# Optimization experiments

Hardware: AMD Instinct MI355X
Metric: run time of the kernel (lower is better)

The kernel has to match this reference:

```python
import jax, jax.numpy as jnp
import numpy as np

NUM_CLASSES = 512


def setup_inputs() -> dict:
    key = jax.random.key(0)
    k1, k2 = jax.random.split(key)
    support_data = jax.random.normal(k1, (2560, 64, 5, 5), dtype=jnp.float32)
    query_data = jax.random.normal(k2, (8192, 64, 5, 5), dtype=jnp.float32)
    # every class 0..511 appears exactly 5 times (sorted, like unique() ordering)
    support_label = (jnp.arange(2560, dtype=jnp.int32) // 5).astype(jnp.int32)
    return {"support_data": support_data, "query_data": query_data,
            "support_label": support_label}


def reference(support_data, query_data, support_label):
    # embedding_net == identity: embeddings are the raw (N, C, H, W) tensors.
    n_q = query_data.shape[0]
    d = support_data.shape[1] * support_data.shape[2] * support_data.shape[3]
    s = support_data.reshape(support_data.shape[0], d)   # [Ns, d]
    q = query_data.reshape(n_q, d)                        # [Nq, d]

    # class-mean prototypes (scatter-mean == per-unique-label mean loop)
    sums = jax.ops.segment_sum(s, support_label, num_segments=NUM_CLASSES)      # [M, d]
    counts = jax.ops.segment_sum(jnp.ones((s.shape[0],), s.dtype),
                                 support_label, num_segments=NUM_CLASSES)       # [M]
    protos = sums / counts[:, None]                                             # [M, d]

    # squared euclidean distance: ||q||^2 + ||p||^2 - 2 q.p  (same math as
    # broadcast (q - p)**2 summed over c,h,w, without the [Nq,M,d] intermediate)
    q2 = jnp.sum(q * q, axis=1, keepdims=True)            # [Nq, 1]
    p2 = jnp.sum(protos * protos, axis=1)                 # [M]
    dist = q2 + p2[None, :] - 2.0 * (q @ protos.T)        # [Nq, M]

    return jax.nn.log_softmax(-dist, axis=1)
```

## Files before the change

### kernel.cpp

```cpp
#include <hip/hip_runtime.h>
#include <hip/hip_bf16.h>
#include <cstdint>
#include <cstddef>

#define NS 2560
#define NQ 8192
#define NC 512
#define DD 1600

typedef __bf16 bf16_t;
typedef __bf16 bf16x4 __attribute__((ext_vector_type(4)));
typedef __bf16 bf16x8 __attribute__((ext_vector_type(8)));
typedef float f32x4 __attribute__((ext_vector_type(4)));

__global__ __launch_bounds__(256) void proto_kernel(
    const float* __restrict__ sup, const int* __restrict__ lab,
    bf16_t* __restrict__ protos, float* __restrict__ p2)
{
    const int m   = blockIdx.x;
    const int tid = threadIdx.x;
    __shared__ int   idxs[32];
    __shared__ int   cnt;
    __shared__ float wsum[4];
    if (tid == 0) cnt = 0;
    __syncthreads();
    for (int i = tid; i < NS; i += 256) {
        if (lab[i] == m) {
            int p = atomicAdd(&cnt, 1);
            if (p < 32) idxs[p] = i;
        }
    }
    __syncthreads();
    int n = cnt < 32 ? cnt : 32;
    if (tid == 0 && n > 1) {
        for (int a = 1; a < n; ++a) {
            int key = idxs[a]; int b = a - 1;
            while (b >= 0 && idxs[b] > key) { idxs[b+1] = idxs[b]; --b; }
            idxs[b+1] = key;
        }
    }
    __syncthreads();

    float acc[7];
    #pragma unroll
    for (int u = 0; u < 7; ++u) acc[u] = 0.f;
    for (int t = 0; t < n; ++t) {
        const float* src = sup + (size_t)idxs[t] * DD;
        #pragma unroll
        for (int u = 0; u < 7; ++u) {
            int j = tid + u * 256;
            if (j < DD) acc[u] += src[j];
        }
    }
    float inv = (n > 0) ? 1.f / (float)n : 0.f;
    float psq = 0.f;
    #pragma unroll
    for (int u = 0; u < 7; ++u) {
        int j = tid + u * 256;
        if (j < DD) {
            float p = acc[u] * inv;
            bf16_t pb = (bf16_t)p;
            protos[(size_t)m * DD + j] = pb;
            float pf = (float)pb;
            psq += pf * pf;
        }
    }
    #pragma unroll
    for (int o = 32; o > 0; o >>= 1) psq += __shfl_xor(psq, o);
    int lane = tid & 63, wid = tid >> 6;
    if (lane == 0) wsum[wid] = psq;
    __syncthreads();
    if (tid == 0) p2[m] = wsum[0] + wsum[1] + wsum[2] + wsum[3];
}

__device__ __forceinline__ void stage_B(const bf16_t* __restrict__ pb,
                                        char* bbuf, int k0, int tid, int wid)
{
    #pragma unroll
    for (int p = 0; p < 4; ++p) {
        int idx  = p * 256 + tid;
        int row  = idx >> 3;
        int gcol = (idx & 7) ^ (row & 7);
        const bf16_t* src = pb + (size_t)row * DD + k0 + gcol * 8;
        char* dst = bbuf + (size_t)(p * 256 + wid * 64) * 16;
        __builtin_amdgcn_global_load_lds(
            (const __attribute__((address_space(1))) void*)src,
            (__attribute__((address_space(3))) void*)dst, 16, 0, 0);
    }
}

__global__ __launch_bounds__(256, 4) void gemm_kernel(
    const float* __restrict__ q, const bf16_t* __restrict__ protos,
    const float* __restrict__ p2, float* __restrict__ out)
{
    __shared__ char smem[20480];

    const int tid  = threadIdx.x;
    const int lane = tid & 63;
    const int wid  = tid >> 6;
    const int r    = lane & 15;
    const int g    = lane >> 4;
    const int m0   = blockIdx.x * 32;
    const int n0   = blockIdx.y * 128;

    const bf16_t* pb = protos + (size_t)n0 * DD;

    float p2c[2];
    #pragma unroll
    for (int ni = 0; ni < 2; ++ni) p2c[ni] = p2[n0 + wid * 32 + ni * 16 + r];

    f32x4 acc[2][2];
    #pragma unroll
    for (int mi = 0; mi < 2; ++mi)
        #pragma unroll
        for (int ni = 0; ni < 2; ++ni)
            acc[mi][ni] = (f32x4){0.f, 0.f, 0.f, 0.f};

    const int ar0 = tid >> 4, ac0 = tid & 15;
    const int ar1 = (256 + tid) >> 4, ac1 = tid & 15;
    const float* ap0 = q + (size_t)(m0 + ar0) * DD + ac0 * 4;
    const float* ap1 = q + (size_t)(m0 + ar1) * DD + ac1 * 4;
    const int ao0 = (ar0 * 128 + ac0 * 8) ^ ((ar0 & 7) << 4);
    const int ao1 = (ar1 * 128 + ac1 * 8) ^ ((ar1 & 7) << 4);

    char* Bs = smem;
    char* As = smem + 16384;

    for (int t = 0; t < 25; ++t) {
        float4 f0 = *(const float4*)(ap0 + t * 64);
        float4 f1 = *(const float4*)(ap1 + t * 64);
        stage_B(pb, Bs, t * 64, tid, wid);
        bf16x4 w0, w1;
        w0[0] = (bf16_t)f0.x; w0[1] = (bf16_t)f0.y;
        w0[2] = (bf16_t)f0.z; w0[3] = (bf16_t)f0.w;
        w1[0] = (bf16_t)f1.x; w1[1] = (bf16_t)f1.y;
        w1[2] = (bf16_t)f1.z; w1[3] = (bf16_t)f1.w;
        *(bf16x4*)(As + ao0) = w0;
        *(bf16x4*)(As + ao1) = w1;
        __syncthreads();

        #pragma unroll
        for (int kk = 0; kk < 2; ++kk) {
            bf16x8 af[2], bfr[2];
            #pragma unroll
            for (int mi = 0; mi < 2; ++mi) {
                int a_r = mi * 16 + r;
                int ab  = (a_r * 128 + kk * 64 + g * 16) ^ ((a_r & 7) << 4);
                af[mi] = *(const bf16x8*)(As + ab);
            }
            #pragma unroll
            for (int ni = 0; ni < 2; ++ni) {
                int c  = wid * 32 + ni * 16 + r;
                int bb = (c * 128 + kk * 64 + g * 16) ^ ((c & 7) << 4);
                bfr[ni] = *(const bf16x8*)(Bs + bb);
            }
            #pragma unroll
            for (int mi = 0; mi < 2; ++mi)
                #pragma unroll
                for (int ni = 0; ni < 2; ++ni)
                    acc[mi][ni] = __builtin_amdgcn_mfma_f32_16x16x32_bf16(
                        af[mi], bfr[ni], acc[mi][ni], 0, 0, 0);
        }
        __syncthreads();
    }

    #pragma unroll
    for (int mi = 0; mi < 2; ++mi) {
        #pragma unroll
        for (int j = 0; j < 4; ++j) {
            size_t rowoff = (size_t)(m0 + mi * 16 + g * 4 + j) * NC + n0;
            #pragma unroll
            for (int ni = 0; ni < 2; ++ni)
                out[rowoff + wid * 32 + ni * 16 + r] =
                    2.f * acc[mi][ni][j] - p2c[ni];
        }
    }
}

__global__ __launch_bounds__(256) void lsm_kernel(float* __restrict__ io)
{
    const int row  = blockIdx.x * 4 + (threadIdx.x >> 6);
    const int lane = threadIdx.x & 63;
    float* p = io + (size_t)row * NC + lane * 8;

    float4 a = *(const float4*)(p);
    float4 b = *(const float4*)(p + 4);
    float v[8] = {a.x, a.y, a.z, a.w, b.x, b.y, b.z, b.w};

    float mx = v[0];
    #pragma unroll
    for (int i = 1; i < 8; ++i) mx = fmaxf(mx, v[i]);
    #pragma unroll
    for (int o = 32; o > 0; o >>= 1) mx = fmaxf(mx, __shfl_xor(mx, o));
    float se = 0.f;
    #pragma unroll
    for (int i = 0; i < 8; ++i) se += expf(v[i] - mx);
    #pragma unroll
    for (int o = 32; o > 0; o >>= 1) se += __shfl_xor(se, o);
    float lz = mx + logf(se);

    float4 o1 = {v[0]-lz, v[1]-lz, v[2]-lz, v[3]-lz};
    float4 o2 = {v[4]-lz, v[5]-lz, v[6]-lz, v[7]-lz};
    *(float4*)(p)     = o1;
    *(float4*)(p + 4) = o2;
}

extern "C" void kernel_launch(void* const* d_in, const int* in_sizes, int n_in,
                              void* d_out, int out_size, void* d_ws, size_t ws_size,
                              hipStream_t stream)
{
    const float* sup = (const float*)d_in[0];
    const float* qry = (const float*)d_in[1];
    const int*   lab = (const int*)d_in[2];
    float* out = (float*)d_out;

    char* ws = (char*)d_ws;
    bf16_t* protos = (bf16_t*)ws;
    float*  p2     = (float*)(ws + 1638400);

    proto_kernel<<<NC, 256, 0, stream>>>(sup, lab, protos, p2);
    gemm_kernel<<<dim3(NQ / 32, 4), 256, 0, stream>>>(qry, protos, p2, out);
    lsm_kernel<<<NQ / 4, 256, 0, stream>>>(out);
}
```

Before: 57.45 us.

## Enlarge GEMM tile to 128x128 with 8 waves and double-buffered LDS prefetch

The GEMM block tile grows from 32x128 to 128x128 using 512 threads arranged as 2x4 waves, each computing a 64x32 sub-tile. This cuts how often the prototype tiles are re-read from global memory. A double-buffered LDS pipeline is added: the next K-slice of A (fp32 converted to bf16) and B (async global_load_lds) is issued before the current slice's MFMAs, so only one barrier per iteration remains. In exchange it uses 64KB of dynamic shared memory and a grid of only 256 blocks, which lowers occupancy and may underfill the CUs.

After: 59.32 us. 3.3% more time.

```diff
diff --git a/kernel.cpp b/kernel.cpp
--- a/kernel.cpp
+++ b/kernel.cpp
@@ -77,101 +77,132 @@
                                         char* bbuf, int k0, int tid, int wid)
 {
     #pragma unroll
-    for (int p = 0; p < 4; ++p) {
-        int idx  = p * 256 + tid;
+    for (int p = 0; p < 2; ++p) {
+        int idx  = p * 512 + tid;
         int row  = idx >> 3;
         int gcol = (idx & 7) ^ (row & 7);
         const bf16_t* src = pb + (size_t)row * DD + k0 + gcol * 8;
-        char* dst = bbuf + (size_t)(p * 256 + wid * 64) * 16;
+        char* dst = bbuf + (size_t)(p * 512 + wid * 64) * 16;
         __builtin_amdgcn_global_load_lds(
             (const __attribute__((address_space(1))) void*)src,
             (__attribute__((address_space(3))) void*)dst, 16, 0, 0);
     }
 }
 
-__global__ __launch_bounds__(256, 4) void gemm_kernel(
+__global__ __launch_bounds__(512, 2) void gemm_kernel(
     const float* __restrict__ q, const bf16_t* __restrict__ protos,
     const float* __restrict__ p2, float* __restrict__ out)
 {
-    __shared__ char smem[20480];
+    extern __shared__ char smem[];
 
     const int tid  = threadIdx.x;
     const int lane = tid & 63;
     const int wid  = tid >> 6;
+    const int wm   = wid >> 2;
+    const int wn   = wid & 3;
     const int r    = lane & 15;
     const int g    = lane >> 4;
-    const int m0   = blockIdx.x * 32;
+    const int m0   = blockIdx.x * 128;
     const int n0   = blockIdx.y * 128;
 
     const bf16_t* pb = protos + (size_t)n0 * DD;
 
     float p2c[2];
     #pragma unroll
-    for (int ni = 0; ni < 2; ++ni) p2c[ni] = p2[n0 + wid * 32 + ni * 16 + r];
-
-    f32x4 acc[2][2];
-    #pragma unroll
-    for (int mi = 0; mi < 2; ++mi)
+    for (int ni = 0; ni < 2; ++ni) p2c[ni] = p2[n0 + wn * 32 + ni * 16 + r];
+
+    f32x4 acc[4][2];
+    #pragma unroll
+    for (int mi = 0; mi < 4; ++mi)
         #pragma unroll
         for (int ni = 0; ni < 2; ++ni)
             acc[mi][ni] = (f32x4){0.f, 0.f, 0.f, 0.f};
 
-    const int ar0 = tid >> 4, ac0 = tid & 15;
-    const int ar1 = (256 + tid) >> 4, ac1 = tid & 15;
-    const float* ap0 = q + (size_t)(m0 + ar0) * DD + ac0 * 4;
-    const float* ap1 = q + (size_t)(m0 + ar1) * DD + ac1 * 4;
-    const int ao0 = (ar0 * 128 + ac0 * 8) ^ ((ar0 & 7) << 4);
-    const int ao1 = (ar1 * 128 + ac1 * 8) ^ ((ar1 & 7) << 4);
-
-    char* Bs = smem;
-    char* As = smem + 16384;
+    const int acg = tid & 15;
+    int          arow[4];
+    const float* ap[4];
+    int          ao[4];
+    #pragma unroll
+    for (int u = 0; u < 4; ++u) {
+        arow[u] = (u * 512 + tid) >> 4;
+        ap[u]   = q + (size_t)(m0 + arow[u]) * DD + acg * 4;
+        ao[u]   = (arow[u] * 128 + acg * 8) ^ ((arow[u] & 7) << 4);
+    }
+
+    {
+        float4 f[4];
+        #pragma unroll
+        for (int u = 0; u < 4; ++u) f[u] = *(const float4*)(ap[u]);
+        stage_B(pb, smem, 0, tid, wid);
+        #pragma unroll
+        for (int u = 0; u < 4; ++u) {
+            bf16x4 w;
+            w[0] = (bf16_t)f[u].x; w[1] = (bf16_t)f[u].y;
+            w[2] = (bf16_t)f[u].z; w[3] = (bf16_t)f[u].w;
+            *(bf16x4*)(smem + 32768 + ao[u]) = w;
+        }
+        __syncthreads();
+    }
 
     for (int t = 0; t < 25; ++t) {
-        float4 f0 = *(const float4*)(ap0 + t * 64);
-        float4 f1 = *(const float4*)(ap1 + t * 64);
-        stage_B(pb, Bs, t * 64, tid, wid);
-        bf16x4 w0, w1;
-        w0[0] = (bf16_t)f0.x; w0[1] = (bf16_t)f0.y;
-        w0[2] = (bf16_t)f0.z; w0[3] = (bf16_t)f0.w;
-        w1[0] = (bf16_t)f1.x; w1[1] = (bf16_t)f1.y;
-        w1[2] = (bf16_t)f1.z; w1[3] = (bf16_t)f1.w;
-        *(bf16x4*)(As + ao0) = w0;
-        *(bf16x4*)(As + ao1) = w1;
-        __syncthreads();
+        const int cur = t & 1;
+        const char* bs  = smem + cur * 16384;
+        char*       bsn = smem + (cur ^ 1) * 16384;
+        const char* as  = smem + 32768 + cur * 16384;
+        char*       asn = smem + 32768 + (cur ^ 1) * 16384;
+        const bool  pre = (t < 24);
+
+        float4 fA[4];
+        if (pre) {
+            #pragma unroll
+            for (int u = 0; u < 4; ++u)
+                fA[u] = *(const float4*)(ap[u] + (t + 1) * 64);
+            stage_B(pb, bsn, (t + 1) * 64, tid, wid);
+        }
 
         #pragma unroll
         for (int kk = 0; kk < 2; ++kk) {
-            bf16x8 af[2], bfr[2];
-            #pragma unroll
-            for (int mi = 0; mi < 2; ++mi) {
-                int a_r = mi * 16 + r;
+            bf16x8 af[4], bfr[2];
+            #pragma unroll
+            for (int mi = 0; mi < 4; ++mi) {
+                int a_r = wm * 64 + mi * 16 + r;
                 int ab  = (a_r * 128 + kk * 64 + g * 16) ^ ((a_r & 7) << 4);
-                af[mi] = *(const bf16x8*)(As + ab);
+                af[mi] = *(const bf16x8*)(as + ab);
             }
             #pragma unroll
             for (int ni = 0; ni < 2; ++ni) {
-                int c  = wid * 32 + ni * 16 + r;
+                int c  = wn * 32 + ni * 16 + r;
                 int bb = (c * 128 + kk * 64 + g * 16) ^ ((c & 7) << 4);
-                bfr[ni] = *(const bf16x8*)(Bs + bb);
+                bfr[ni] = *(const bf16x8*)(bs + bb);
             }
             #pragma unroll
-            for (int mi = 0; mi < 2; ++mi)
+            for (int mi = 0; mi < 4; ++mi)
                 #pragma unroll
                 for (int ni = 0; ni < 2; ++ni)
                     acc[mi][ni] = __builtin_amdgcn_mfma_f32_16x16x32_bf16(
                         af[mi], bfr[ni], acc[mi][ni], 0, 0, 0);
         }
+
+        if (pre) {
+            #pragma unroll
+            for (int u = 0; u < 4; ++u) {
+                bf16x4 w;
+                w[0] = (bf16_t)fA[u].x; w[1] = (bf16_t)fA[u].y;
+                w[2] = (bf16_t)fA[u].z; w[3] = (bf16_t)fA[u].w;
+                *(bf16x4*)(asn + ao[u]) = w;
+            }
+        }
         __syncthreads();
     }
 
     #pragma unroll
-    for (int mi = 0; mi < 2; ++mi) {
+    for (int mi = 0; mi < 4; ++mi) {
         #pragma unroll
         for (int j = 0; j < 4; ++j) {
-            size_t rowoff = (size_t)(m0 + mi * 16 + g * 4 + j) * NC + n0;
+            size_t rowoff = (size_t)(m0 + wm * 64 + mi * 16 + g * 4 + j) * NC + n0;
             #pragma unroll
             for (int ni = 0; ni < 2; ++ni)
-                out[rowoff + wid * 32 + ni * 16 + r] =
+                out[rowoff + wn * 32 + ni * 16 + r] =
                     2.f * acc[mi][ni][j] - p2c[ni];
         }
     }
@@ -218,7 +249,11 @@
     bf16_t* protos = (bf16_t*)ws;
     float*  p2     = (float*)(ws + 1638400);
 
+    const int smem_bytes = 65536;
+    hipFuncSetAttribute(reinterpret_cast<const void*>(gemm_kernel),
+                        hipFuncAttributeMaxDynamicSharedMemorySize, smem_bytes);
+
     proto_kernel<<<NC, 256, 0, stream>>>(sup, lab, protos, p2);
-    gemm_kernel<<<dim3(NQ / 32, 4), 256, 0, stream>>>(qry, protos, p2, out);
+    gemm_kernel<<<dim3(NQ / 128, NC / 128), 512, smem_bytes, stream>>>(qry, protos, p2, out);
     lsm_kernel<<<NQ / 4, 256, 0, stream>>>(out);
 }
```
